# Kernel optimization log

Measured on AMD Instinct MI355X. Metric: run time of the kernel, lower is better.

Reference implementation:

```python
import jax, jax.numpy as jnp
import numpy as np

N = 512 * 512       # height * width nodes
C = 200             # spectral channels
HID = 64            # hide
E = 2_097_152       # edges per graph (avg degree 8)
L = 2               # layers_count
CLS = 16            # class_count
EPS = 1e-5


def _bn(x, g, b):
    # BatchNorm1d in training mode: batch stats over node dim (biased var)
    m = x.mean(0)
    v = x.var(0)
    return (x - m) * jax.lax.rsqrt(v + EPS) * g + b


def _ln(x, g, b):
    m = x.mean(-1, keepdims=True)
    v = x.var(-1, keepdims=True)
    return (x - m) * jax.lax.rsqrt(v + EPS) * g + b


def setup_inputs() -> dict:
    key = jax.random.key(0)
    ks = jax.random.split(key, 12)
    inp = {
        "x": jax.random.normal(ks[0], (N, C), jnp.float32),
        "row_att": jax.random.uniform(ks[1], (E, 1), jnp.float32),
        "col_att": jax.random.uniform(ks[2], (E, 1), jnp.float32),
        "prelin_W": jax.random.normal(ks[3], (C, HID), jnp.float32) * (1.0 / np.sqrt(C)),
        "prelin_b": jnp.zeros((HID,), jnp.float32),
        "bn0_g": jnp.ones((HID,), jnp.float32),
        "bn0_b": jnp.zeros((HID,), jnp.float32),
        "ln_g": jnp.ones((L, HID), jnp.float32),
        "ln_b": jnp.zeros((L, HID), jnp.float32),
        "Wrv": jax.random.normal(ks[4], (L, HID, HID), jnp.float32) * (1.0 / np.sqrt(HID)),
        "brv": jnp.zeros((L, HID), jnp.float32),
        "Wcv": jax.random.normal(ks[5], (L, HID, HID), jnp.float32) * (1.0 / np.sqrt(HID)),
        "bcv": jnp.zeros((L, HID), jnp.float32),
        "bn_g": jnp.ones((L, HID), jnp.float32),
        "bn_b": jnp.zeros((L, HID), jnp.float32),
        "sm_W": jax.random.normal(ks[6], (HID, CLS), jnp.float32) * (1.0 / np.sqrt(HID)),
        "sm_b": jnp.zeros((CLS,), jnp.float32),
        "rowsrc": jax.random.randint(ks[7], (E,), 0, N, jnp.int32),
        "rowdst": jax.random.randint(ks[8], (E,), 0, N, jnp.int32),
        "colsrc": jax.random.randint(ks[9], (E,), 0, N, jnp.int32),
        "coldst": jax.random.randint(ks[10], (E,), 0, N, jnp.int32),
    }
    return inp


def reference(x, row_att, col_att, prelin_W, prelin_b, bn0_g, bn0_b,
              ln_g, ln_b, Wrv, brv, Wcv, bcv, bn_g, bn_b, sm_W, sm_b,
              rowsrc, rowdst, colsrc, coldst):
    # stem: prelin + BN
    h = _bn(x @ prelin_W + prelin_b, bn0_g, bn0_b)  # [N, HID]
    for i in range(L):
        xn = _ln(h, ln_g[i], ln_b[i])               # [N, HID]
        rowv = xn @ Wrv[i] + brv[i]
        colv = xn @ Wcv[i] + bcv[i]
        # gather by dst, weight by precomputed attention, scatter-sum to src
        rowagg = rowv[rowdst] * row_att             # [E, HID]
        colagg = colv[coldst] * col_att             # [E, HID]
        rowout = jax.ops.segment_sum(rowagg, rowsrc, num_segments=N)
        colout = jax.ops.segment_sum(colagg, colsrc, num_segments=N)
        out = rowout + colout + xn                  # concat=False -> sum, + residual
        h = jax.nn.leaky_relu(_bn(out, bn_g[i], bn_b[i]), 0.01)
    logits = h @ sm_W + sm_b                        # [N, CLS]
    return jax.nn.softmax(logits, axis=-1)
```

## Files before the change

kernel.cpp:

```cpp
#include <hip/hip_runtime.h>
#include <math.h>

#define NN   262144
#define CIN  200
#define EE   2097152
#define NB   (2*NN)
#define BKN  2048
#define NBKT 256
#define CAP  18176
#define EPSV 1e-5f

typedef __bf16 bf16x8 __attribute__((ext_vector_type(8)));
typedef float  f32x4  __attribute__((ext_vector_type(4)));

__device__ __forceinline__ unsigned short f2bf(float f) {
    unsigned int u = __float_as_uint(f);
    unsigned int r = (u + 0x7fffu + ((u >> 16) & 1u)) >> 16;
    return (unsigned short)r;
}
__device__ __forceinline__ float bf2f(unsigned short u) {
    return __uint_as_float(((unsigned int)u) << 16);
}

__global__ __launch_bounds__(256) void w_convert_stem(
    const float* __restrict__ W, unsigned short* __restrict__ wbufS)
{
    int idx = blockIdx.x * 256 + threadIdx.x;
    if (idx >= 28 * 64 * 8) return;
    int e    = idx & 7;
    int lane = (idx >> 3) & 63;
    int f    = idx >> 9;
    int t    = f & 3;
    int kb   = f >> 2;
    int k    = kb * 32 + ((lane >> 4) & 3) * 8 + e;
    float w  = (k < CIN) ? W[k * 64 + t * 16 + (lane & 15)] : 0.f;
    wbufS[idx] = f2bf(w);
}

__global__ __launch_bounds__(256) void stem_mfma(
    const float* __restrict__ x, const unsigned short* __restrict__ wbS,
    const float* __restrict__ bias, unsigned short* __restrict__ t,
    float* __restrict__ stats)
{
    const int lane = threadIdx.x & 63;
    const int wloc = threadIdx.x >> 6;
    const int lo   = lane & 15;
    const int hi   = lane >> 4;
    const int n0   = blockIdx.x * 64 + wloc * 16;

    float bb4[4];
#pragma unroll
    for (int tt = 0; tt < 4; ++tt) bb4[tt] = bias[tt * 16 + lo];

    f32x4 acc[4];
#pragma unroll
    for (int tt = 0; tt < 4; ++tt) acc[tt] = (f32x4){0.f, 0.f, 0.f, 0.f};

    const bf16x8* wb = (const bf16x8*)wbS;
    const float* xrow = x + (size_t)(n0 + lo) * CIN;

#pragma unroll
    for (int kb = 0; kb < 7; ++kb) {
        union { bf16x8 b; unsigned short u[8]; } A;
        if (kb < 6 || hi == 0) {
            const float* px = xrow + kb * 32 + hi * 8;
            float4 u0 = *(const float4*)px;
            float4 u1 = *(const float4*)(px + 4);
            A.u[0] = f2bf(u0.x); A.u[1] = f2bf(u0.y);
            A.u[2] = f2bf(u0.z); A.u[3] = f2bf(u0.w);
            A.u[4] = f2bf(u1.x); A.u[5] = f2bf(u1.y);
            A.u[6] = f2bf(u1.z); A.u[7] = f2bf(u1.w);
        } else {
#pragma unroll
            for (int i = 0; i < 8; ++i) A.u[i] = 0;
        }
#pragma unroll
        for (int tt = 0; tt < 4; ++tt)
            acc[tt] = __builtin_amdgcn_mfma_f32_16x16x32_bf16(
                A.b, wb[(kb * 4 + tt) * 64 + lane], acc[tt], 0, 0, 0);
    }

    float ss[4] = {0.f, 0.f, 0.f, 0.f}, ss2[4] = {0.f, 0.f, 0.f, 0.f};
#pragma unroll
    for (int tt = 0; tt < 4; ++tt) {
        const int col = tt * 16 + lo;
#pragma unroll
        for (int r = 0; r < 4; ++r) {
            const int n = n0 + hi * 4 + r;
            float v = acc[tt][r] + bb4[tt];
            t[(size_t)n * 64 + col] = f2bf(v);
            ss[tt] += v;
            ss2[tt] += v * v;
        }
    }

#pragma unroll
    for (int tt = 0; tt < 4; ++tt) {
        ss[tt]  += __shfl_xor(ss[tt], 16);  ss[tt]  += __shfl_xor(ss[tt], 32);
        ss2[tt] += __shfl_xor(ss2[tt], 16); ss2[tt] += __shfl_xor(ss2[tt], 32);
    }
    __shared__ float ls[4][64], ls2[4][64];
    if (lo == lane) {
#pragma unroll
        for (int tt = 0; tt < 4; ++tt) {
            ls[wloc][tt * 16 + lane]  = ss[tt];
            ls2[wloc][tt * 16 + lane] = ss2[tt];
        }
    }
    __syncthreads();
    if (threadIdx.x < 64) {
        int ch = threadIdx.x;
        atomicAdd(&stats[ch],      ls[0][ch] + ls[1][ch] + ls[2][ch] + ls[3][ch]);
        atomicAdd(&stats[64 + ch], ls2[0][ch] + ls2[1][ch] + ls2[2][ch] + ls2[3][ch]);
    }
}

__global__ void finalize_bn(const float* __restrict__ stats,
                            const float* __restrict__ g, const float* __restrict__ b,
                            float* __restrict__ ac)
{
    int c = threadIdx.x;
    float mean = stats[c] * (1.f / NN);
    float var  = stats[64 + c] * (1.f / NN) - mean * mean;
    float rstd = rsqrtf(var + EPSV);
    float a = g[c] * rstd;
    ac[c]      = a;
    ac[64 + c] = b[c] - mean * a;
}

template <int RELU>
__global__ __launch_bounds__(256) void ln_kernel(
    const unsigned short* __restrict__ u, const float* __restrict__ ac,
    const float* __restrict__ lng, const float* __restrict__ lnb,
    unsigned short* __restrict__ xnb)
{
    const int lane = threadIdx.x & 63;
    const int wid  = (blockIdx.x * 256 + threadIdx.x) >> 6;
    const int nw   = (gridDim.x * 256) >> 6;
    const float a  = ac[lane],  c0 = ac[64 + lane];
    const float g  = lng[lane], bl = lnb[lane];

    for (int row = wid; row < NN; row += nw) {
        float v = bf2f(u[(size_t)row * 64 + lane]);
        v = v * a + c0;
        if (RELU) v = (v > 0.f) ? v : 0.01f * v;
        float s = v;
#pragma unroll
        for (int off = 32; off > 0; off >>= 1) s += __shfl_xor(s, off);
        float mean = s * (1.f / 64.f);
        float d = v - mean;
        float s2 = d * d;
#pragma unroll
        for (int off = 32; off > 0; off >>= 1) s2 += __shfl_xor(s2, off);
        float rstd = rsqrtf(s2 * (1.f / 64.f) + EPSV);
        float o = d * rstd * g + bl;
        xnb[(size_t)row * 64 + lane] = f2bf(o);
    }
}

__global__ __launch_bounds__(256) void hist_kernel(
    const int* __restrict__ rowsrc, const int* __restrict__ colsrc,
    int* __restrict__ cnt)
{
    for (int i = blockIdx.x * 256 + threadIdx.x; i < EE; i += gridDim.x * 256) {
        atomicAdd(&cnt[rowsrc[i]], 1);
        atomicAdd(&cnt[NN + colsrc[i]], 1);
    }
}

__global__ __launch_bounds__(256) void scan1_kernel(
    const int* __restrict__ cnt, int* __restrict__ bsum)
{
    const int t = threadIdx.x;
    const int base = blockIdx.x * 1024 + t * 4;
    int s = cnt[base] + cnt[base + 1] + cnt[base + 2] + cnt[base + 3];
    __shared__ int sm[256];
    sm[t] = s;
    __syncthreads();
    for (int off = 1; off < 256; off <<= 1) {
        int v = (t >= off) ? sm[t - off] : 0;
        __syncthreads();
        sm[t] += v;
        __syncthreads();
    }
    if (t == 255) bsum[blockIdx.x] = sm[255];
}

__global__ __launch_bounds__(512) void scan2_kernel(
    const int* __restrict__ bsum, int* __restrict__ bpre, int* __restrict__ ptr)
{
    const int t = threadIdx.x;
    __shared__ int sm[512];
    int orig = bsum[t];
    sm[t] = orig;
    __syncthreads();
    for (int off = 1; off < 512; off <<= 1) {
        int v = (t >= off) ? sm[t - off] : 0;
        __syncthreads();
        sm[t] += v;
        __syncthreads();
    }
    bpre[t] = sm[t] - orig;
    if (t == 0) ptr[NB] = 2 * EE;
}

__global__ __launch_bounds__(256) void scan3_kernel(
    const int* __restrict__ cnt, const int* __restrict__ bpre,
    int* __restrict__ ptr, int* __restrict__ cursor)
{
    const int t = threadIdx.x;
    const int base = blockIdx.x * 1024 + t * 4;
    int c0 = cnt[base], c1 = cnt[base + 1], c2 = cnt[base + 2], c3 = cnt[base + 3];
    int tsum = c0 + c1 + c2 + c3;
    __shared__ int sm[256];
    sm[t] = tsum;
    __syncthreads();
    for (int off = 1; off < 256; off <<= 1) {
        int v = (t >= off) ? sm[t - off] : 0;
        __syncthreads();
        sm[t] += v;
        __syncthreads();
    }
    int p = bpre[blockIdx.x] + sm[t] - tsum;
    ptr[base] = p;     cursor[base] = p;     p += c0;
    ptr[base + 1] = p; cursor[base + 1] = p; p += c1;
    ptr[base + 2] = p; cursor[base + 2] = p; p += c2;
    ptr[base + 3] = p; cursor[base + 3] = p;
}

__global__ void winit_kernel(const int* __restrict__ ptr, int* __restrict__ wcur)
{
    int t = threadIdx.x;
    wcur[t] = ptr[t * BKN];
}

__global__ __launch_bounds__(256) void partA_kernel(
    const int* __restrict__ rowsrc, const int* __restrict__ rowdst,
    const float* __restrict__ ratt,
    const int* __restrict__ colsrc, const int* __restrict__ coldst,
    const float* __restrict__ catt,
    int* __restrict__ wcur,
    long long* __restrict__ psd, float* __restrict__ patt)
{
    __shared__ int hcnt[NBKT], hbase[NBKT];
    const int tid = threadIdx.x;

    for (long long t0 = (long long)blockIdx.x * 1024; t0 < 2LL * EE;
         t0 += (long long)gridDim.x * 1024) {
        hcnt[tid] = 0;
        __syncthreads();

        int w[4], rank[4], dstv[4], sfl[4];
        float attv[4];
#pragma unroll
        for (int u = 0; u < 4; ++u) {
            long long i = t0 + u * 256 + tid;
            if (i < 2LL * EE) {
                bool isrow = i < EE;
                long long j = isrow ? i : i - EE;
                int s   = isrow ? __builtin_nontemporal_load(&rowsrc[j])
                                : __builtin_nontemporal_load(&colsrc[j]);
                dstv[u] = isrow ? __builtin_nontemporal_load(&rowdst[j])
                                : __builtin_nontemporal_load(&coldst[j]);
                attv[u] = isrow ? __builtin_nontemporal_load(&ratt[j])
                                : __builtin_nontemporal_load(&catt[j]);
                sfl[u]  = (isrow ? 0 : NN) + s;
                w[u]    = sfl[u] >> 11;
                rank[u] = atomicAdd(&hcnt[w[u]], 1);
            } else {
                w[u] = -1;
            }
        }
        __syncthreads();
        hbase[tid] = atomicAdd(&wcur[tid], hcnt[tid]);
        __syncthreads();
#pragma unroll
        for (int u = 0; u < 4; ++u) {
            if (w[u] >= 0) {
                int pos = hbase[w[u]] + rank[u];
                psd[pos]  = ((long long)sfl[u] << 32) | (unsigned int)dstv[u];
                patt[pos] = attv[u];
            }
        }
        __syncthreads();
    }
}

__global__ __launch_bounds__(256) void partB_lds(
    const int* __restrict__ ptr,
    const long long* __restrict__ psd, const float* __restrict__ patt,
    int2* __restrict__ edges)
{
    __shared__ int lcnt[BKN];
    __shared__ long long lrec[CAP];
    __shared__ int sm[256];
    const int tid  = threadIdx.x;
    const int b    = blockIdx.x;
    const int nb0  = b * BKN;
    const int base = ptr[nb0];
    const int end  = ptr[nb0 + BKN];
    const int cnt  = end - base;

    for (int i = tid; i < BKN; i += 256) lcnt[i] = 0;
    __syncthreads();

    for (int i = tid; i < cnt; i += 256) {
        int s = (int)(psd[base + i] >> 32);
        atomicAdd(&lcnt[s - nb0], 1);
    }
    __syncthreads();

    int loc[8], tsum = 0;
#pragma unroll
    for (int j = 0; j < 8; ++j) { loc[j] = lcnt[tid * 8 + j]; tsum += loc[j]; }
    sm[tid] = tsum;
    __syncthreads();
    for (int off = 1; off < 256; off <<= 1) {
        int v = (tid >= off) ? sm[tid - off] : 0;
        __syncthreads();
        sm[tid] += v;
        __syncthreads();
    }
    int run = sm[tid] - tsum;
#pragma unroll
    for (int j = 0; j < 8; ++j) { lcnt[tid * 8 + j] = run; run += loc[j]; }
    __syncthreads();

    for (int i = tid; i < cnt; i += 256) {
        long long q = psd[base + i];
        float    a = patt[base + i];
        int s = (int)(q >> 32);
        int d = (int)(q & 0xffffffffLL);
        int off = atomicAdd(&lcnt[s - nb0], 1);
        long long rec = ((long long)__float_as_int(a) << 32) | (unsigned int)d;
        if (off < CAP) lrec[off] = rec;
        else edges[base + off] = make_int2(d, __float_as_int(a));
    }
    __syncthreads();

    const int lim = (cnt < CAP) ? cnt : CAP;
    for (int i = tid; i < lim; i += 256) {
        long long rec = lrec[i];
        edges[base + i] = make_int2((int)(rec & 0xffffffffLL), (int)(rec >> 32));
    }
}

__global__ __launch_bounds__(256) void gather_kernel(
    const unsigned short* __restrict__ xnb,
    const int* __restrict__ ptr, const int2* __restrict__ edges,
    unsigned short* __restrict__ rxb, unsigned short* __restrict__ cxb,
    float2* __restrict__ attsum)
{
    const int lane = threadIdx.x & 63;
    const int wid  = (blockIdx.x * 256 + threadIdx.x) >> 6;
    const int nw   = (gridDim.x * 256) >> 6;
    const int HALF = NN / 2;

    for (int n = wid; n < HALF; n += nw) {
        const int m = n + HALF;
        const int i0 = ptr[n],      e0 = ptr[n + 1];
        const int i1 = ptr[NN + n], e1 = ptr[NN + n + 1];
        const int i2 = ptr[m],      e2 = ptr[m + 1];
        const int i3 = ptr[NN + m], e3 = ptr[NN + m + 1];
        const int len0 = e0 - i0, len1 = e1 - i1, len2 = e2 - i2, len3 = e3 - i3;
        int maxlen = max(max(len0, len1), max(len2, len3));

        float rx0 = 0.f, cx0 = 0.f, rx1 = 0.f, cx1 = 0.f;
        float ras0 = 0.f, cas0 = 0.f, ras1 = 0.f, cas1 = 0.f;

#pragma unroll 2
        for (int k = 0; k < maxlen; ++k) {
            int j0 = min(i0 + ((k < len0) ? k : 0), 2 * EE - 1);
            int j1 = min(i1 + ((k < len1) ? k : 0), 2 * EE - 1);
            int j2 = min(i2 + ((k < len2) ? k : 0), 2 * EE - 1);
            int j3 = min(i3 + ((k < len3) ? k : 0), 2 * EE - 1);
            int2 p0 = edges[j0];
            int2 p1 = edges[j1];
            int2 p2 = edges[j2];
            int2 p3 = edges[j3];
            float v0 = bf2f(xnb[(size_t)p0.x * 64 + lane]);
            float v1 = bf2f(xnb[(size_t)p1.x * 64 + lane]);
            float v2 = bf2f(xnb[(size_t)p2.x * 64 + lane]);
            float v3 = bf2f(xnb[(size_t)p3.x * 64 + lane]);
            float a0 = (k < len0) ? __int_as_float(p0.y) : 0.f;
            float a1 = (k < len1) ? __int_as_float(p1.y) : 0.f;
            float a2 = (k < len2) ? __int_as_float(p2.y) : 0.f;
            float a3 = (k < len3) ? __int_as_float(p3.y) : 0.f;
            rx0 = fmaf(v0, a0, rx0); ras0 += a0;
            cx0 = fmaf(v1, a1, cx0); cas0 += a1;
            rx1 = fmaf(v2, a2, rx1); ras1 += a2;
            cx1 = fmaf(v3, a3, cx1); cas1 += a3;
        }

        rxb[(size_t)n * 64 + lane] = f2bf(rx0);
        cxb[(size_t)n * 64 + lane] = f2bf(cx0);
        rxb[(size_t)m * 64 + lane] = f2bf(rx1);
        cxb[(size_t)m * 64 + lane] = f2bf(cx1);
        if (lane == 0) {
            attsum[n] = make_float2(ras0, cas0);
            attsum[m] = make_float2(ras1, cas1);
        }
    }
}

__global__ __launch_bounds__(256) void w_convert(
    const float* __restrict__ Wrv, const float* __restrict__ Wcv,
    unsigned short* __restrict__ wbuf)
{
    int idx = blockIdx.x * 256 + threadIdx.x;
    int e    = idx & 7;
    int lane = (idx >> 3) & 63;
    int t    = (idx >> 9) & 3;
    int kb   = (idx >> 11) & 1;
    int m    = (idx >> 12) & 1;
    int L    = (idx >> 13) & 1;
    const float* W = (m ? Wcv : Wrv) + L * 4096;
    float w = W[(kb * 32 + ((lane >> 4) & 3) * 8 + e) * 64 + t * 16 + (lane & 15)];
    wbuf[idx] = f2bf(w);
}

__global__ __launch_bounds__(256) void gemv_mfma(
    const unsigned short* __restrict__ rxb, const unsigned short* __restrict__ cxb,
    const unsigned short* __restrict__ xnb, const float2* __restrict__ attsum,
    const unsigned short* __restrict__ wb16,
    const float* __restrict__ br, const float* __restrict__ bc,
    unsigned short* __restrict__ out, float* __restrict__ stats)
{
    const int lane = threadIdx.x & 63;
    const int wloc = threadIdx.x >> 6;
    const int wid  = (blockIdx.x * 256 + threadIdx.x) >> 6;
    const int nw   = (gridDim.x * 256) >> 6;
    const int lo   = lane & 15;
    const int hi   = lane >> 4;

    const bf16x8* wb = (const bf16x8*)wb16;
    bf16x8 bfr[2][2][4];
#pragma unroll
    for (int m = 0; m < 2; ++m)
#pragma unroll
        for (int kb = 0; kb < 2; ++kb)
#pragma unroll
            for (int t = 0; t < 4; ++t)
                bfr[m][kb][t] = wb[((m * 2 + kb) * 4 + t) * 64 + lane];

    float brv4[4], bcv4[4];
#pragma unroll
    for (int t = 0; t < 4; ++t) {
        brv4[t] = br[t * 16 + lo];
        bcv4[t] = bc[t * 16 + lo];
    }

    float ss[4] = {0.f, 0.f, 0.f, 0.f}, ss2[4] = {0.f, 0.f, 0.f, 0.f};
    const bf16x8* ra = (const bf16x8*)rxb;
    const bf16x8* ca = (const bf16x8*)cxb;

    for (int tile = wid; tile < NN / 16; tile += nw) {
        const int n0 = tile * 16;
        const int arow = n0 + lo;
        bf16x8 a0 = ra[arow * 8 + hi];
        bf16x8 a1 = ra[arow * 8 + 4 + hi];
        bf16x8 c0 = ca[arow * 8 + hi];
        bf16x8 c1 = ca[arow * 8 + 4 + hi];
        float2 an[4];
#pragma unroll
        for (int r = 0; r < 4; ++r) an[r] = attsum[n0 + hi * 4 + r];

#pragma unroll
        for (int t = 0; t < 4; ++t) {
            f32x4 acc = {0.f, 0.f, 0.f, 0.f};
            acc = __builtin_amdgcn_mfma_f32_16x16x32_bf16(a0, bfr[0][0][t], acc, 0, 0, 0);
            acc = __builtin_amdgcn_mfma_f32_16x16x32_bf16(a1, bfr[0][1][t], acc, 0, 0, 0);
            acc = __builtin_amdgcn_mfma_f32_16x16x32_bf16(c0, bfr[1][0][t], acc, 0, 0, 0);
            acc = __builtin_amdgcn_mfma_f32_16x16x32_bf16(c1, bfr[1][1][t], acc, 0, 0, 0);
            const int col = t * 16 + lo;
#pragma unroll
            for (int r = 0; r < 4; ++r) {
                const int n = n0 + hi * 4 + r;
                float v = acc[r] + bf2f(xnb[(size_t)n * 64 + col])
                        + an[r].x * brv4[t] + an[r].y * bcv4[t];
                out[(size_t)n * 64 + col] = f2bf(v);
                ss[t] += v;
                ss2[t] += v * v;
            }
        }
    }

#pragma unroll
    for (int t = 0; t < 4; ++t) {
        ss[t]  += __shfl_xor(ss[t], 16);  ss[t]  += __shfl_xor(ss[t], 32);
        ss2[t] += __shfl_xor(ss2[t], 16); ss2[t] += __shfl_xor(ss2[t], 32);
    }
    __shared__ float ls[4][64], ls2[4][64];
    if (lo == lane) {
#pragma unroll
        for (int t = 0; t < 4; ++t) {
            ls[wloc][t * 16 + lane]  = ss[t];
            ls2[wloc][t * 16 + lane] = ss2[t];
        }
    }
    __syncthreads();
    if (threadIdx.x < 64) {
        int ch = threadIdx.x;
        atomicAdd(&stats[ch],      ls[0][ch] + ls[1][ch] + ls[2][ch] + ls[3][ch]);
        atomicAdd(&stats[64 + ch], ls2[0][ch] + ls2[1][ch] + ls2[2][ch] + ls2[3][ch]);
    }
}

__global__ __launch_bounds__(256) void out_kernel(
    const unsigned short* __restrict__ agg, const float* __restrict__ ac,
    const float* __restrict__ smW, const float* __restrict__ smb,
    float* __restrict__ out)
{
    __shared__ float sW[64 * 16];
    for (int i = threadIdx.x; i < 64 * 16; i += 256) sW[i] = smW[i];
    __syncthreads();
    const int j = threadIdx.x & 15;
    const int rloc = threadIdx.x >> 4;
    const float bj = smb[j];
    for (int row = blockIdx.x * 16 + rloc; row < NN; row += gridDim.x * 16) {
        float acc = bj;
#pragma unroll
        for (int k = 0; k < 64; ++k) {
            float v = bf2f(agg[(size_t)row * 64 + k]);
            v = v * ac[k] + ac[64 + k];
            v = (v > 0.f) ? v : 0.01f * v;
            acc = fmaf(v, sW[k * 16 + j], acc);
        }
        float m = acc;
#pragma unroll
        for (int off = 8; off > 0; off >>= 1) m = fmaxf(m, __shfl_xor(m, off));
        float e = expf(acc - m);
        float ssum = e;
#pragma unroll
        for (int off = 8; off > 0; off >>= 1) ssum += __shfl_xor(ssum, off);
        out[(size_t)row * 16 + j] = e / ssum;
    }
}

extern "C" void kernel_launch(void* const* d_in, const int* in_sizes, int n_in,
                              void* d_out, int out_size, void* d_ws, size_t ws_size,
                              hipStream_t stream)
{
    const float* x        = (const float*)d_in[0];
    const float* row_att  = (const float*)d_in[1];
    const float* col_att  = (const float*)d_in[2];
    const float* prelin_W = (const float*)d_in[3];
    const float* prelin_b = (const float*)d_in[4];
    const float* bn0_g    = (const float*)d_in[5];
    const float* bn0_b    = (const float*)d_in[6];
    const float* ln_g     = (const float*)d_in[7];
    const float* ln_b     = (const float*)d_in[8];
    const float* Wrv      = (const float*)d_in[9];
    const float* brv      = (const float*)d_in[10];
    const float* Wcv      = (const float*)d_in[11];
    const float* bcv      = (const float*)d_in[12];
    const float* bn_g     = (const float*)d_in[13];
    const float* bn_b     = (const float*)d_in[14];
    const float* sm_W     = (const float*)d_in[15];
    const float* sm_b     = (const float*)d_in[16];
    const int*   rowsrc   = (const int*)d_in[17];
    const int*   rowdst   = (const int*)d_in[18];
    const int*   colsrc   = (const int*)d_in[19];
    const int*   coldst   = (const int*)d_in[20];
    float* out = (float*)d_out;

    const size_t NH = (size_t)NN * 64;
    char* extra = (char*)d_ws;
    unsigned short* A   = (unsigned short*)extra; extra += NH * sizeof(short);
    unsigned short* xnb = (unsigned short*)extra; extra += NH * sizeof(short);
    unsigned short* rxb = (unsigned short*)extra; extra += NH * sizeof(short);
    unsigned short* cxb = (unsigned short*)extra; extra += NH * sizeof(short);
    float2* attsum = (float2*)extra;              extra += (size_t)NN * sizeof(float2);
    float* stats  = (float*)extra;                extra += 3 * 128 * sizeof(float);
    float* ac     = (float*)extra;                extra += 3 * 128 * sizeof(float);
    unsigned short* wbuf  = (unsigned short*)extra; extra += 16384 * sizeof(short);
    unsigned short* wbufS = (unsigned short*)extra; extra += 14336 * sizeof(short);
    int*   bsum   = (int*)extra;                  extra += 512 * sizeof(int);
    int*   bpre   = (int*)extra;                  extra += 512 * sizeof(int);
    int*   ptr    = (int*)extra;                  extra += (NB + 1) * sizeof(int);
    int*   counts = (int*)extra;                  extra += NB * sizeof(int);
    int*   cursor = (int*)extra;                  extra += NB * sizeof(int);
    int*   wcur   = (int*)extra;                  extra += NBKT * sizeof(int);
    int2*  edges  = (int2*)extra;                 extra += 2 * (size_t)EE * sizeof(int2);

    long long* psd = (long long*)rxb;
    float*    patt = (float*)cxb;

    hipMemsetAsync(stats, 0, 3 * 128 * sizeof(float), stream);
    hipMemsetAsync(counts, 0, NB * sizeof(int), stream);

    hist_kernel<<<2048, 256, 0, stream>>>(rowsrc, colsrc, counts);
    scan1_kernel<<<512, 256, 0, stream>>>(counts, bsum);
    scan2_kernel<<<1, 512, 0, stream>>>(bsum, bpre, ptr);
    scan3_kernel<<<512, 256, 0, stream>>>(counts, bpre, ptr, cursor);
    winit_kernel<<<1, 256, 0, stream>>>(ptr, wcur);
    partA_kernel<<<1024, 256, 0, stream>>>(rowsrc, rowdst, row_att,
                                           colsrc, coldst, col_att,
                                           wcur, psd, patt);
    partB_lds<<<NBKT, 256, 0, stream>>>(ptr, psd, patt, edges);
    w_convert<<<64, 256, 0, stream>>>(Wrv, Wcv, wbuf);
    w_convert_stem<<<56, 256, 0, stream>>>(prelin_W, wbufS);

    stem_mfma<<<NN / 64, 256, 0, stream>>>(x, wbufS, prelin_b, A, stats);
    finalize_bn<<<1, 64, 0, stream>>>(stats, bn0_g, bn0_b, ac);

    ln_kernel<0><<<4096, 256, 0, stream>>>(A, ac, ln_g, ln_b, xnb);
    gather_kernel<<<8192, 256, 0, stream>>>(xnb, ptr, edges, rxb, cxb, attsum);
    gemv_mfma<<<2048, 256, 0, stream>>>(rxb, cxb, xnb, attsum, wbuf,
                                        brv, bcv, A, stats + 128);
    finalize_bn<<<1, 64, 0, stream>>>(stats + 128, bn_g, bn_b, ac + 128);

    ln_kernel<1><<<4096, 256, 0, stream>>>(A, ac + 128, ln_g + 64, ln_b + 64, xnb);
    gather_kernel<<<8192, 256, 0, stream>>>(xnb, ptr, edges, rxb, cxb, attsum);
    gemv_mfma<<<2048, 256, 0, stream>>>(rxb, cxb, xnb, attsum, wbuf + 8192,
                                        brv + 64, bcv + 64, A, stats + 256);
    finalize_bn<<<1, 64, 0, stream>>>(stats + 256, bn_g + 64, bn_b + 64, ac + 256);

    out_kernel<<<2048, 256, 0, stream>>>(A, ac + 256, sm_W, sm_b, out);
}
```

Measured before the change: 1.222 ms.

## Replace per-node histogram and three-pass scan with per-bucket counts and partB-computed row pointers

```diff
diff --git a/kernel.cpp b/kernel.cpp
--- a/kernel.cpp
+++ b/kernel.cpp
@@ -22,19 +22,33 @@
     return __uint_as_float(((unsigned int)u) << 16);
 }
 
-__global__ __launch_bounds__(256) void w_convert_stem(
-    const float* __restrict__ W, unsigned short* __restrict__ wbufS)
+__global__ __launch_bounds__(256) void w_all(
+    const float* __restrict__ Wrv, const float* __restrict__ Wcv,
+    const float* __restrict__ Wstem,
+    unsigned short* __restrict__ wbuf, unsigned short* __restrict__ wbufS)
 {
     int idx = blockIdx.x * 256 + threadIdx.x;
-    if (idx >= 28 * 64 * 8) return;
-    int e    = idx & 7;
-    int lane = (idx >> 3) & 63;
-    int f    = idx >> 9;
-    int t    = f & 3;
-    int kb   = f >> 2;
-    int k    = kb * 32 + ((lane >> 4) & 3) * 8 + e;
-    float w  = (k < CIN) ? W[k * 64 + t * 16 + (lane & 15)] : 0.f;
-    wbufS[idx] = f2bf(w);
+    if (idx < 16384) {
+        int e    = idx & 7;
+        int lane = (idx >> 3) & 63;
+        int t    = (idx >> 9) & 3;
+        int kb   = (idx >> 11) & 1;
+        int m    = (idx >> 12) & 1;
+        int L    = (idx >> 13) & 1;
+        const float* W = (m ? Wcv : Wrv) + L * 4096;
+        float w = W[(kb * 32 + ((lane >> 4) & 3) * 8 + e) * 64 + t * 16 + (lane & 15)];
+        wbuf[idx] = f2bf(w);
+    } else if (idx < 16384 + 14336) {
+        int j    = idx - 16384;
+        int e    = j & 7;
+        int lane = (j >> 3) & 63;
+        int f    = j >> 9;
+        int t    = f & 3;
+        int kb   = f >> 2;
+        int k    = kb * 32 + ((lane >> 4) & 3) * 8 + e;
+        float w  = (k < CIN) ? Wstem[k * 64 + t * 16 + (lane & 15)] : 0.f;
+        wbufS[j] = f2bf(w);
+    }
 }
 
 __global__ __launch_bounds__(256) void stem_mfma(
@@ -158,24 +172,30 @@
     }
 }
 
-__global__ __launch_bounds__(256) void hist_kernel(
+__global__ __launch_bounds__(256) void bhist_kernel(
     const int* __restrict__ rowsrc, const int* __restrict__ colsrc,
-    int* __restrict__ cnt)
-{
+    int* __restrict__ bcnt)
+{
+    __shared__ int h[NBKT];
+    h[threadIdx.x] = 0;
+    __syncthreads();
     for (int i = blockIdx.x * 256 + threadIdx.x; i < EE; i += gridDim.x * 256) {
-        atomicAdd(&cnt[rowsrc[i]], 1);
-        atomicAdd(&cnt[NN + colsrc[i]], 1);
-    }
-}
-
-__global__ __launch_bounds__(256) void scan1_kernel(
-    const int* __restrict__ cnt, int* __restrict__ bsum)
+        atomicAdd(&h[rowsrc[i] >> 11], 1);
+        atomicAdd(&h[128 + (colsrc[i] >> 11)], 1);
+    }
+    __syncthreads();
+    int v = h[threadIdx.x];
+    if (v) atomicAdd(&bcnt[threadIdx.x], v);
+}
+
+__global__ __launch_bounds__(256) void bscan_kernel(
+    const int* __restrict__ bcnt, int* __restrict__ bbase,
+    int* __restrict__ wcur, int* __restrict__ ptr)
 {
     const int t = threadIdx.x;
-    const int base = blockIdx.x * 1024 + t * 4;
-    int s = cnt[base] + cnt[base + 1] + cnt[base + 2] + cnt[base + 3];
     __shared__ int sm[256];
-    sm[t] = s;
+    int orig = bcnt[t];
+    sm[t] = orig;
     __syncthreads();
     for (int off = 1; off < 256; off <<= 1) {
         int v = (t >= off) ? sm[t - off] : 0;
@@ -183,55 +203,10 @@
         sm[t] += v;
         __syncthreads();
     }
-    if (t == 255) bsum[blockIdx.x] = sm[255];
-}
-
-__global__ __launch_bounds__(512) void scan2_kernel(
-    const int* __restrict__ bsum, int* __restrict__ bpre, int* __restrict__ ptr)
-{
-    const int t = threadIdx.x;
-    __shared__ int sm[512];
-    int orig = bsum[t];
-    sm[t] = orig;
-    __syncthreads();
-    for (int off = 1; off < 512; off <<= 1) {
-        int v = (t >= off) ? sm[t - off] : 0;
-        __syncthreads();
-        sm[t] += v;
-        __syncthreads();
-    }
-    bpre[t] = sm[t] - orig;
-    if (t == 0) ptr[NB] = 2 * EE;
-}
-
-__global__ __launch_bounds__(256) void scan3_kernel(
-    const int* __restrict__ cnt, const int* __restrict__ bpre,
-    int* __restrict__ ptr, int* __restrict__ cursor)
-{
-    const int t = threadIdx.x;
-    const int base = blockIdx.x * 1024 + t * 4;
-    int c0 = cnt[base], c1 = cnt[base + 1], c2 = cnt[base + 2], c3 = cnt[base + 3];
-    int tsum = c0 + c1 + c2 + c3;
-    __shared__ int sm[256];
-    sm[t] = tsum;
-    __syncthreads();
-    for (int off = 1; off < 256; off <<= 1) {
-        int v = (t >= off) ? sm[t - off] : 0;
-        __syncthreads();
-        sm[t] += v;
-        __syncthreads();
-    }
-    int p = bpre[blockIdx.x] + sm[t] - tsum;
-    ptr[base] = p;     cursor[base] = p;     p += c0;
-    ptr[base + 1] = p; cursor[base + 1] = p; p += c1;
-    ptr[base + 2] = p; cursor[base + 2] = p; p += c2;
-    ptr[base + 3] = p; cursor[base + 3] = p;
-}
-
-__global__ void winit_kernel(const int* __restrict__ ptr, int* __restrict__ wcur)
-{
-    int t = threadIdx.x;
-    wcur[t] = ptr[t * BKN];
+    int excl = sm[t] - orig;
+    bbase[t] = excl;
+    wcur[t]  = excl;
+    if (t == 255) { bbase[256] = 2 * EE; ptr[NB] = 2 * EE; }
 }
 
 __global__ __launch_bounds__(256) void partA_kernel(
@@ -286,36 +261,36 @@
     }
 }
 
-__global__ __launch_bounds__(256) void partB_lds(
-    const int* __restrict__ ptr,
+__global__ __launch_bounds__(512) void partB_lds(
+    const int* __restrict__ bbase,
     const long long* __restrict__ psd, const float* __restrict__ patt,
-    int2* __restrict__ edges)
+    int* __restrict__ ptr, int2* __restrict__ edges)
 {
     __shared__ int lcnt[BKN];
     __shared__ long long lrec[CAP];
-    __shared__ int sm[256];
+    __shared__ int sm[512];
     const int tid  = threadIdx.x;
     const int b    = blockIdx.x;
     const int nb0  = b * BKN;
-    const int base = ptr[nb0];
-    const int end  = ptr[nb0 + BKN];
+    const int base = bbase[b];
+    const int end  = bbase[b + 1];
     const int cnt  = end - base;
 
-    for (int i = tid; i < BKN; i += 256) lcnt[i] = 0;
-    __syncthreads();
-
-    for (int i = tid; i < cnt; i += 256) {
+    for (int i = tid; i < BKN; i += 512) lcnt[i] = 0;
+    __syncthreads();
+
+    for (int i = tid; i < cnt; i += 512) {
         int s = (int)(psd[base + i] >> 32);
         atomicAdd(&lcnt[s - nb0], 1);
     }
     __syncthreads();
 
-    int loc[8], tsum = 0;
-#pragma unroll
-    for (int j = 0; j < 8; ++j) { loc[j] = lcnt[tid * 8 + j]; tsum += loc[j]; }
+    int loc[4], tsum = 0;
+#pragma unroll
+    for (int j = 0; j < 4; ++j) { loc[j] = lcnt[tid * 4 + j]; tsum += loc[j]; }
     sm[tid] = tsum;
     __syncthreads();
-    for (int off = 1; off < 256; off <<= 1) {
+    for (int off = 1; off < 512; off <<= 1) {
         int v = (tid >= off) ? sm[tid - off] : 0;
         __syncthreads();
         sm[tid] += v;
@@ -323,10 +298,14 @@
     }
     int run = sm[tid] - tsum;
 #pragma unroll
-    for (int j = 0; j < 8; ++j) { lcnt[tid * 8 + j] = run; run += loc[j]; }
-    __syncthreads();
-
-    for (int i = tid; i < cnt; i += 256) {
+    for (int j = 0; j < 4; ++j) {
+        lcnt[tid * 4 + j] = run;
+        ptr[nb0 + tid * 4 + j] = base + run;
+        run += loc[j];
+    }
+    __syncthreads();
+
+    for (int i = tid; i < cnt; i += 512) {
         long long q = psd[base + i];
         float    a = patt[base + i];
         int s = (int)(q >> 32);
@@ -339,7 +318,7 @@
     __syncthreads();
 
     const int lim = (cnt < CAP) ? cnt : CAP;
-    for (int i = tid; i < lim; i += 256) {
+    for (int i = tid; i < lim; i += 512) {
         long long rec = lrec[i];
         edges[base + i] = make_int2((int)(rec & 0xffffffffLL), (int)(rec >> 32));
     }
@@ -403,22 +382,6 @@
     }
 }
 
-__global__ __launch_bounds__(256) void w_convert(
-    const float* __restrict__ Wrv, const float* __restrict__ Wcv,
-    unsigned short* __restrict__ wbuf)
-{
-    int idx = blockIdx.x * 256 + threadIdx.x;
-    int e    = idx & 7;
-    int lane = (idx >> 3) & 63;
-    int t    = (idx >> 9) & 3;
-    int kb   = (idx >> 11) & 1;
-    int m    = (idx >> 12) & 1;
-    int L    = (idx >> 13) & 1;
-    const float* W = (m ? Wcv : Wrv) + L * 4096;
-    float w = W[(kb * 32 + ((lane >> 4) & 3) * 8 + e) * 64 + t * 16 + (lane & 15)];
-    wbuf[idx] = f2bf(w);
-}
-
 __global__ __launch_bounds__(256) void gemv_mfma(
     const unsigned short* __restrict__ rxb, const unsigned short* __restrict__ cxb,
     const unsigned short* __restrict__ xnb, const float2* __restrict__ attsum,
@@ -572,34 +535,27 @@
     unsigned short* cxb = (unsigned short*)extra; extra += NH * sizeof(short);
     float2* attsum = (float2*)extra;              extra += (size_t)NN * sizeof(float2);
     float* stats  = (float*)extra;                extra += 3 * 128 * sizeof(float);
+    int*   bcnt   = (int*)extra;                  extra += NBKT * sizeof(int);
     float* ac     = (float*)extra;                extra += 3 * 128 * sizeof(float);
     unsigned short* wbuf  = (unsigned short*)extra; extra += 16384 * sizeof(short);
     unsigned short* wbufS = (unsigned short*)extra; extra += 14336 * sizeof(short);
-    int*   bsum   = (int*)extra;                  extra += 512 * sizeof(int);
-    int*   bpre   = (int*)extra;                  extra += 512 * sizeof(int);
+    int*   bbase  = (int*)extra;                  extra += (NBKT + 1) * sizeof(int);
+    int*   wcur   = (int*)extra;                  extra += NBKT * sizeof(int);
     int*   ptr    = (int*)extra;                  extra += (NB + 1) * sizeof(int);
-    int*   counts = (int*)extra;                  extra += NB * sizeof(int);
-    int*   cursor = (int*)extra;                  extra += NB * sizeof(int);
-    int*   wcur   = (int*)extra;                  extra += NBKT * sizeof(int);
     int2*  edges  = (int2*)extra;                 extra += 2 * (size_t)EE * sizeof(int2);
 
     long long* psd = (long long*)rxb;
     float*    patt = (float*)cxb;
 
-    hipMemsetAsync(stats, 0, 3 * 128 * sizeof(float), stream);
-    hipMemsetAsync(counts, 0, NB * sizeof(int), stream);
-
-    hist_kernel<<<2048, 256, 0, stream>>>(rowsrc, colsrc, counts);
-    scan1_kernel<<<512, 256, 0, stream>>>(counts, bsum);
-    scan2_kernel<<<1, 512, 0, stream>>>(bsum, bpre, ptr);
-    scan3_kernel<<<512, 256, 0, stream>>>(counts, bpre, ptr, cursor);
-    winit_kernel<<<1, 256, 0, stream>>>(ptr, wcur);
+    hipMemsetAsync(stats, 0, (3 * 128 + NBKT) * sizeof(float), stream);
+
+    bhist_kernel<<<1024, 256, 0, stream>>>(rowsrc, colsrc, bcnt);
+    bscan_kernel<<<1, 256, 0, stream>>>(bcnt, bbase, wcur, ptr);
     partA_kernel<<<1024, 256, 0, stream>>>(rowsrc, rowdst, row_att,
                                            colsrc, coldst, col_att,
                                            wcur, psd, patt);
-    partB_lds<<<NBKT, 256, 0, stream>>>(ptr, psd, patt, edges);
-    w_convert<<<64, 256, 0, stream>>>(Wrv, Wcv, wbuf);
-    w_convert_stem<<<56, 256, 0, stream>>>(prelin_W, wbufS);
+    partB_lds<<<NBKT, 512, 0, stream>>>(bbase, psd, patt, ptr, edges);
+    w_all<<<120, 256, 0, stream>>>(Wrv, Wcv, prelin_W, wbuf, wbufS);
 
     stem_mfma<<<NN / 64, 256, 0, stream>>>(x, wbufS, prelin_b, A, stats);
     finalize_bn<<<1, 64, 0, stream>>>(stats, bn0_g, bn0_b, ac);
```

Result: faster. 1.051 ms (-14.0%).
